# Optimization experiments

Measured on AMD Instinct MI355X. Metric: run time of the kernel, lower is better.

The kernel has to match this reference:

```python
import jax, jax.numpy as jnp
import numpy as np

ALPHA = 0.4
EPS = 1e-5


def setup_inputs() -> dict:
    key = jax.random.key(0)
    features = jax.random.normal(key, (32, 1024, 512), dtype=jnp.float32)
    return {"features": features}


def reference(features):
    B, dim, M = features.shape
    # x_pow2 = x @ x^T / (2M), shape [B, dim, dim]
    x_pow2 = jnp.einsum('bdm,bem->bde', features, features) / (2.0 * M)
    # I_M.bmm(x_pow2*I) broadcasts the diagonal along rows; (x_pow2*I).bmm(I_M) along cols
    diag = jnp.diagonal(x_pow2, axis1=1, axis2=2)  # [B, dim]
    dcov = diag[:, None, :] + diag[:, :, None] - 2.0 * x_pow2
    dcov = jnp.maximum(dcov, 0.0)
    dcov = jnp.power(dcov + EPS, ALPHA)
    # double-centering: the ones/dim matmuls are exactly row/col/total means
    row_mean = jnp.mean(dcov, axis=2, keepdims=True)   # dcov.bmm(I_M/dim)
    col_mean = jnp.mean(dcov, axis=1, keepdims=True)   # (I_M/dim).bmm(dcov)
    tot_mean = jnp.mean(dcov, axis=(1, 2), keepdims=True)
    out = dcov - row_mean - col_mean + tot_mean        # [B, dim, dim]
    # triuvec: upper-triangular (incl. diagonal) entries, row-major order
    idx = np.nonzero(np.triu(np.ones((dim, dim), dtype=np.float32)).reshape(-1))[0]
    return out.reshape(B, dim * dim)[:, idx]
```

## Files before the change

### kernel.cpp

```cpp
#include <hip/hip_runtime.h>
#include <hip/hip_bf16.h>

#define B_ 32
#define D_ 1024
#define M_ 512
#define OUTROW 524800
#define ALPHA_ 0.4f
#define EPS_ 1e-5f

typedef __bf16 bf16x8 __attribute__((ext_vector_type(8)));
typedef float f32x4 __attribute__((ext_vector_type(4)));

__global__ __launch_bounds__(256) void prep_kernel(
    const float* __restrict__ feat, __bf16* __restrict__ featbf,
    float* __restrict__ diag, float* __restrict__ rowsum,
    float* __restrict__ totals)
{
    if (blockIdx.x < 128) {
        rowsum[blockIdx.x * 256 + threadIdx.x] = 0.0f;
        if (blockIdx.x == 0 && threadIdx.x < B_) totals[threadIdx.x] = 0.0f;
    }

    const int w = threadIdx.x >> 6, l = threadIdx.x & 63;
    const int row = blockIdx.x * 4 + w;
    const float4* fp = (const float4*)(feat + (size_t)row * M_);
    float4 v0 = fp[l * 2];
    float4 v1 = fp[l * 2 + 1];
    bf16x8 h;
    h[0] = (__bf16)v0.x; h[1] = (__bf16)v0.y; h[2] = (__bf16)v0.z; h[3] = (__bf16)v0.w;
    h[4] = (__bf16)v1.x; h[5] = (__bf16)v1.y; h[6] = (__bf16)v1.z; h[7] = (__bf16)v1.w;
    *(bf16x8*)(featbf + (size_t)row * M_ + l * 8) = h;
    float s = v0.x*v0.x + v0.y*v0.y + v0.z*v0.z + v0.w*v0.w
            + v1.x*v1.x + v1.y*v1.y + v1.z*v1.z + v1.w*v1.w;
    #pragma unroll
    for (int off = 32; off; off >>= 1) s += __shfl_down(s, off);
    if (l == 0) diag[row] = s * (1.0f / (2.0f * M_));
}

__global__ __launch_bounds__(256, 3) void gram_kernel(
    const __bf16* __restrict__ feat, const float* __restrict__ diag,
    float* __restrict__ out, float* __restrict__ rowsum,
    float* __restrict__ totals)
{
    __shared__ __bf16 As[3][512 * 8];
    __shared__ __bf16 Bs[3][512 * 8];

    const int t = threadIdx.x;
    const int w = t >> 6, l = t & 63;
    const int quad = l >> 4, l15 = l & 15;

    const int L = blockIdx.x;
    const int xcd = L & 7;
    const int slot = L >> 3;
    const int b = xcd + 8 * (slot / 36);
    int u = slot % 36, ti = 0;
    while (u >= 8 - ti) { u -= 8 - ti; ti++; }
    const int tj = ti + u;
    const bool diagTile = (ti == tj);

    const __bf16* Ab = feat + (size_t)b * (D_ * M_) + (size_t)ti * 128 * M_;
    const __bf16* Bb = feat + (size_t)b * (D_ * M_) + (size_t)tj * 128 * M_;

    const int wm = w >> 1, wn = w & 1;

    const int gi0 = ti * 128 + wm * 64;
    const int gj0 = tj * 128 + wn * 64;
    const float* diagB = diag + b * D_;
    float di[4][4], dj[4];
    #pragma unroll
    for (int mi = 0; mi < 4; ++mi)
        #pragma unroll
        for (int r = 0; r < 4; ++r)
            di[mi][r] = diagB[gi0 + mi * 16 + quad * 4 + r];
    #pragma unroll
    for (int nj = 0; nj < 4; ++nj)
        dj[nj] = diagB[gj0 + nj * 16 + l15];

    f32x4 acc[4][4] = {};

    auto stage = [&](int s, int sb) {
        const int koff = s * 32;
        #pragma unroll
        for (int it = 0; it < 2; ++it) {
            const int idx = it * 256 + t;
            const int row = idx >> 2;
            const int cg = (idx & 3) ^ ((row >> 1) & 3);
            const __bf16* ga = Ab + row * M_ + koff + cg * 8;
            const __bf16* gb = Bb + row * M_ + koff + cg * 8;
            __builtin_amdgcn_global_load_lds(
                (const __attribute__((address_space(1))) void*)ga,
                (__attribute__((address_space(3))) void*)(&As[sb][(it * 256 + w * 64) * 8]),
                16, 0, 0);
            __builtin_amdgcn_global_load_lds(
                (const __attribute__((address_space(1))) void*)gb,
                (__attribute__((address_space(3))) void*)(&Bs[sb][(it * 256 + w * 64) * 8]),
                16, 0, 0);
        }
    };

    stage(0, 0);
    stage(1, 1);
    int rb = 0, sn = 2;
    for (int k0 = 0; k0 < 16; ++k0) {
        if (k0 < 15) asm volatile("s_waitcnt vmcnt(4)" ::: "memory");
        else         asm volatile("s_waitcnt vmcnt(0)" ::: "memory");
        __builtin_amdgcn_s_barrier();
        __builtin_amdgcn_sched_barrier(0);
        if (k0 + 2 < 16) stage(k0 + 2, sn);

        bf16x8 af[4], bfr[4];
        #pragma unroll
        for (int mi = 0; mi < 4; ++mi) {
            const int row = wm * 64 + mi * 16 + l15;
            af[mi] = *(const bf16x8*)(&As[rb][(row * 4 + (quad ^ ((row >> 1) & 3))) * 8]);
        }
        #pragma unroll
        for (int nj = 0; nj < 4; ++nj) {
            const int row = wn * 64 + nj * 16 + l15;
            bfr[nj] = *(const bf16x8*)(&Bs[rb][(row * 4 + (quad ^ ((row >> 1) & 3))) * 8]);
        }
        __builtin_amdgcn_s_setprio(1);
        #pragma unroll
        for (int mi = 0; mi < 4; ++mi)
            #pragma unroll
            for (int nj = 0; nj < 4; ++nj)
                acc[mi][nj] = __builtin_amdgcn_mfma_f32_16x16x32_bf16(
                    af[mi], bfr[nj], acc[mi][nj], 0, 0, 0);
        __builtin_amdgcn_s_setprio(0);
        rb = (rb == 2) ? 0 : rb + 1;
        sn = (sn == 2) ? 0 : sn + 1;
    }

    float* outB = out + (size_t)b * OUTROW;
    float rs[4][4] = {};
    float cs[4] = {};
    float wt = 0.f;
    const float invK = 1.0f / 512.0f;

    #pragma unroll
    for (int mi = 0; mi < 4; ++mi) {
        #pragma unroll
        for (int nj = 0; nj < 4; ++nj) {
            const f32x4 a = acc[mi][nj];
            const int j = gj0 + nj * 16 + l15;
            #pragma unroll
            for (int r = 0; r < 4; ++r) {
                const int i = gi0 + mi * 16 + quad * 4 + r;
                float d = di[mi][r] + dj[nj] - a[r] * invK;
                if (i == j) d = 0.0f;
                d = fmaxf(d, 0.0f);
                const float p = __builtin_exp2f(ALPHA_ * __builtin_log2f(d + EPS_));
                rs[mi][r] += p;
                cs[nj] += p;
                wt += p;
                if (!diagTile || j >= i)
                    outB[(size_t)i * D_ - ((size_t)i * (i + 1)) / 2 + j] = p;
            }
        }
    }

    #pragma unroll
    for (int mi = 0; mi < 4; ++mi) {
        #pragma unroll
        for (int r = 0; r < 4; ++r) {
            float v = rs[mi][r];
            v += __shfl_xor(v, 1); v += __shfl_xor(v, 2);
            v += __shfl_xor(v, 4); v += __shfl_xor(v, 8);
            if (l15 == 0)
                unsafeAtomicAdd(&rowsum[b * D_ + gi0 + mi * 16 + quad * 4 + r], v);
        }
    }
    if (!diagTile) {
        #pragma unroll
        for (int nj = 0; nj < 4; ++nj) {
            float v = cs[nj];
            v += __shfl_xor(v, 16); v += __shfl_xor(v, 32);
            if (quad == 0)
                unsafeAtomicAdd(&rowsum[b * D_ + gj0 + nj * 16 + l15], v);
        }
    }
    float v = wt;
    #pragma unroll
    for (int off = 32; off; off >>= 1) v += __shfl_down(v, off);
    if (l == 0) unsafeAtomicAdd(&totals[b], diagTile ? v : 2.0f * v);
}

__global__ __launch_bounds__(256) void center_kernel(
    float* __restrict__ out, const float* __restrict__ rowsum,
    const float* __restrict__ totals)
{
    const int tot4 = OUTROW / 4;
    const float invD = 1.0f / (float)D_;
    const int gsz = gridDim.x * 256;

    for (int g = blockIdx.x * 256 + threadIdx.x; g < B_ * tot4; g += gsz) {
        const int b = g / tot4;
        const int e = (g - b * tot4) * 4;
        const float* rsB = rowsum + b * D_;
        const float tm = totals[b] * (1.0f / ((float)D_ * (float)D_));
        float* outB = out + (size_t)b * OUTROW;

        const float disc = 4198401.0f - 8.0f * (float)e;
        int i = (int)((2049.0f - __builtin_sqrtf(disc)) * 0.5f);
        if (i > 1023) i = 1023;
        if (i < 0) i = 0;
        while (i * (2049 - i) / 2 > e) --i;
        while ((i + 1) * (2049 - (i + 1)) / 2 <= e) ++i;

        float4 v = *(float4*)(outB + e);
        float r[4] = {v.x, v.y, v.z, v.w};
        int ii = i;
        int si = ii * (2049 - ii) / 2;
        int sn = (ii + 1) * (2049 - ii - 1) / 2;
        #pragma unroll
        for (int q = 0; q < 4; ++q) {
            const int eq = e + q;
            while (eq >= sn) {
                ++ii; si = sn;
                sn = (ii + 1) * (2049 - ii - 1) / 2;
            }
            const int j = eq - si + ii;
            r[q] = r[q] - (rsB[ii] + rsB[j]) * invD + tm;
        }
        v.x = r[0]; v.y = r[1]; v.z = r[2]; v.w = r[3];
        *(float4*)(outB + e) = v;
    }
}

extern "C" void kernel_launch(void* const* d_in, const int* in_sizes, int n_in,
                              void* d_out, int out_size, void* d_ws, size_t ws_size,
                              hipStream_t stream) {
    const float* feat = (const float*)d_in[0];
    float* out = (float*)d_out;

    char* ws = (char*)d_ws;
    __bf16* featbf = (__bf16*)ws;
    float* diag    = (float*)(ws + 33554432);
    float* rowsum  = (float*)(ws + 33554432 + 131072);
    float* totals  = (float*)(ws + 33554432 + 262144);

    prep_kernel<<<dim3((B_ * D_) / 4), dim3(256), 0, stream>>>(feat, featbf, diag,
                                                               rowsum, totals);
    gram_kernel<<<dim3(36 * B_), dim3(256), 0, stream>>>(featbf, diag, out, rowsum, totals);
    center_kernel<<<dim3(2048), dim3(256), 0, stream>>>(out, rowsum, totals);
}
```

Baseline: 203.7 us.

## Fuse centering into gram kernel via per-batch completion counter spin-wait

Removes the separate centering kernel launch. Each gram block increments a per-batch done counter, spins until all 36 tiles of its batch are finished, then centers its own slice of that batch's packed output. This saves a launch and lets centering of early batches overlap gram work of later ones. It relies on all 36 blocks of a batch being co-resident to avoid deadlock (1152 blocks at 3 per CU fit on 256 CUs), and spinning blocks hold CU slots.

```diff
diff --git a/kernel.cpp b/kernel.cpp
--- a/kernel.cpp
+++ b/kernel.cpp
@@ -14,11 +14,14 @@
 __global__ __launch_bounds__(256) void prep_kernel(
     const float* __restrict__ feat, __bf16* __restrict__ featbf,
     float* __restrict__ diag, float* __restrict__ rowsum,
-    float* __restrict__ totals)
+    float* __restrict__ totals, int* __restrict__ done)
 {
     if (blockIdx.x < 128) {
         rowsum[blockIdx.x * 256 + threadIdx.x] = 0.0f;
-        if (blockIdx.x == 0 && threadIdx.x < B_) totals[threadIdx.x] = 0.0f;
+        if (blockIdx.x == 0 && threadIdx.x < B_) {
+            totals[threadIdx.x] = 0.0f;
+            done[threadIdx.x] = 0;
+        }
     }
 
     const int w = threadIdx.x >> 6, l = threadIdx.x & 63;
@@ -40,7 +43,7 @@
 __global__ __launch_bounds__(256, 3) void gram_kernel(
     const __bf16* __restrict__ feat, const float* __restrict__ diag,
     float* __restrict__ out, float* __restrict__ rowsum,
-    float* __restrict__ totals)
+    float* __restrict__ totals, int* __restrict__ done)
 {
     __shared__ __bf16 As[3][512 * 8];
     __shared__ __bf16 Bs[3][512 * 8];
@@ -53,7 +56,8 @@
     const int xcd = L & 7;
     const int slot = L >> 3;
     const int b = xcd + 8 * (slot / 36);
-    int u = slot % 36, ti = 0;
+    const int rank = slot % 36;
+    int u = rank, ti = 0;
     while (u >= 8 - ti) { u -= 8 - ti; ti++; }
     const int tj = ti + u;
     const bool diagTile = (ti == tj);
@@ -183,47 +187,54 @@
     #pragma unroll
     for (int off = 32; off; off >>= 1) v += __shfl_down(v, off);
     if (l == 0) unsafeAtomicAdd(&totals[b], diagTile ? v : 2.0f * v);
-}
-
-__global__ __launch_bounds__(256) void center_kernel(
-    float* __restrict__ out, const float* __restrict__ rowsum,
-    const float* __restrict__ totals)
-{
-    const int tot4 = OUTROW / 4;
-    const float invD = 1.0f / (float)D_;
-    const int gsz = gridDim.x * 256;
-
-    for (int g = blockIdx.x * 256 + threadIdx.x; g < B_ * tot4; g += gsz) {
-        const int b = g / tot4;
-        const int e = (g - b * tot4) * 4;
+
+    __threadfence();
+    __syncthreads();
+    if (t == 0) {
+        __hip_atomic_fetch_add(&done[b], 1, __ATOMIC_RELEASE,
+                               __HIP_MEMORY_SCOPE_AGENT);
+        while (__hip_atomic_load(&done[b], __ATOMIC_ACQUIRE,
+                                 __HIP_MEMORY_SCOPE_AGENT) < 36)
+            __builtin_amdgcn_s_sleep(8);
+    }
+    __syncthreads();
+
+    {
+        const int tot4 = OUTROW / 4;
+        const int chunk = 3645;
+        const int g0 = rank * chunk;
+        const int g1 = (g0 + chunk < tot4) ? g0 + chunk : tot4;
+        const float invD = 1.0f / (float)D_;
         const float* rsB = rowsum + b * D_;
         const float tm = totals[b] * (1.0f / ((float)D_ * (float)D_));
-        float* outB = out + (size_t)b * OUTROW;
-
-        const float disc = 4198401.0f - 8.0f * (float)e;
-        int i = (int)((2049.0f - __builtin_sqrtf(disc)) * 0.5f);
-        if (i > 1023) i = 1023;
-        if (i < 0) i = 0;
-        while (i * (2049 - i) / 2 > e) --i;
-        while ((i + 1) * (2049 - (i + 1)) / 2 <= e) ++i;
-
-        float4 v = *(float4*)(outB + e);
-        float r[4] = {v.x, v.y, v.z, v.w};
-        int ii = i;
-        int si = ii * (2049 - ii) / 2;
-        int sn = (ii + 1) * (2049 - ii - 1) / 2;
-        #pragma unroll
-        for (int q = 0; q < 4; ++q) {
-            const int eq = e + q;
-            while (eq >= sn) {
-                ++ii; si = sn;
-                sn = (ii + 1) * (2049 - ii - 1) / 2;
+
+        for (int g = g0 + t; g < g1; g += 256) {
+            const int e = g * 4;
+            const float disc = 4198401.0f - 8.0f * (float)e;
+            int i = (int)((2049.0f - __builtin_sqrtf(disc)) * 0.5f);
+            if (i > 1023) i = 1023;
+            if (i < 0) i = 0;
+            while (i * (2049 - i) / 2 > e) --i;
+            while ((i + 1) * (2049 - (i + 1)) / 2 <= e) ++i;
+
+            float4 vv = *(float4*)(outB + e);
+            float r[4] = {vv.x, vv.y, vv.z, vv.w};
+            int ii = i;
+            int si = ii * (2049 - ii) / 2;
+            int sn2 = (ii + 1) * (2049 - ii - 1) / 2;
+            #pragma unroll
+            for (int q = 0; q < 4; ++q) {
+                const int eq = e + q;
+                while (eq >= sn2) {
+                    ++ii; si = sn2;
+                    sn2 = (ii + 1) * (2049 - ii - 1) / 2;
+                }
+                const int j = eq - si + ii;
+                r[q] = r[q] - (rsB[ii] + rsB[j]) * invD + tm;
             }
-            const int j = eq - si + ii;
-            r[q] = r[q] - (rsB[ii] + rsB[j]) * invD + tm;
-        }
-        v.x = r[0]; v.y = r[1]; v.z = r[2]; v.w = r[3];
-        *(float4*)(outB + e) = v;
+            vv.x = r[0]; vv.y = r[1]; vv.z = r[2]; vv.w = r[3];
+            *(float4*)(outB + e) = vv;
+        }
     }
 }
 
@@ -238,9 +249,10 @@
     float* diag    = (float*)(ws + 33554432);
     float* rowsum  = (float*)(ws + 33554432 + 131072);
     float* totals  = (float*)(ws + 33554432 + 262144);
+    int*   done    = (int*)  (ws + 33554432 + 262144 + 128);
 
     prep_kernel<<<dim3((B_ * D_) / 4), dim3(256), 0, stream>>>(feat, featbf, diag,
-                                                               rowsum, totals);
-    gram_kernel<<<dim3(36 * B_), dim3(256), 0, stream>>>(featbf, diag, out, rowsum, totals);
-    center_kernel<<<dim3(2048), dim3(256), 0, stream>>>(out, rowsum, totals);
+                                                               rowsum, totals, done);
+    gram_kernel<<<dim3(36 * B_), dim3(256), 0, stream>>>(featbf, diag, out, rowsum,
+                                                         totals, done);
 }
```

New measurement: 689.4 us. 3.38x slower.
